# Kernel optimization log

Hardware: AMD Instinct MI355X
Metric: run time of the kernel (lower is better)

Reference implementation:

```python
import jax, jax.numpy as jnp
import numpy as np

D_MODEL = 1024
N_HEADS = 16
D_FF = 4096
LN_EPS = 1e-5


def _layer_norm(x, g, b):
    m = jnp.mean(x, axis=-1, keepdims=True)
    v = jnp.mean((x - m) ** 2, axis=-1, keepdims=True)
    return (x - m) / jnp.sqrt(v + LN_EPS) * g + b


def setup_inputs() -> dict:
    key = jax.random.key(0)
    ks = jax.random.split(key, 16)
    s = 0.02
    d, dff = D_MODEL, D_FF
    return {
        "x": jax.random.normal(ks[0], (8, 1000, d), dtype=jnp.float32),
        # weights stored as (d_in, d_out); applied via x @ W
        "wq": jax.random.normal(ks[1], (d, d), dtype=jnp.float32) * s,
        "wk": jax.random.normal(ks[2], (d, d), dtype=jnp.float32) * s,
        "wv": jax.random.normal(ks[3], (d, d), dtype=jnp.float32) * s,
        "wo": jax.random.normal(ks[4], (d, d), dtype=jnp.float32) * s,
        "bo": jnp.zeros((d,), dtype=jnp.float32),
        "w1": jax.random.normal(ks[5], (d, dff), dtype=jnp.float32) * s,
        "b1": jnp.zeros((dff,), dtype=jnp.float32),
        "w2": jax.random.normal(ks[6], (dff, d), dtype=jnp.float32) * s,
        "b2": jnp.zeros((d,), dtype=jnp.float32),
        "g1": jnp.ones((d,), dtype=jnp.float32),
        "beta1": jnp.zeros((d,), dtype=jnp.float32),
        "g2": jnp.ones((d,), dtype=jnp.float32),
        "beta2": jnp.zeros((d,), dtype=jnp.float32),
    }


def reference(x, wq, wk, wv, wo, bo, w1, b1, w2, b2, g1, beta1, g2, beta2):
    B, S, D = x.shape
    H = N_HEADS
    dk = D // H

    # --- pre-norm attention ---
    h = _layer_norm(x, g1, beta1)
    q = (h @ wq).reshape(B, S, H, dk)
    k = (h @ wk).reshape(B, S, H, dk)
    v = (h @ wv).reshape(B, S, H, dk)
    scores = jnp.einsum('bqhd,bkhd->bhqk', q, k) / jnp.sqrt(jnp.float32(dk))
    mask = jnp.tril(jnp.ones((S, S), dtype=bool))  # causal
    scores = jnp.where(mask, scores, -jnp.inf)
    attn = jax.nn.softmax(scores, axis=-1)
    attended = jnp.einsum('bhqk,bkhd->bqhd', attn, v).reshape(B, S, D)
    x = x + attended @ wo + bo

    # --- pre-norm FFN (exact GELU, matching torch F.gelu default) ---
    h2 = _layer_norm(x, g2, beta2)
    ff = jax.nn.gelu(h2 @ w1 + b1, approximate=False) @ w2 + b2
    return x + ff
```

## Files before the change

### kernel.cpp

```cpp
#include <hip/hip_runtime.h>
#include <hip/hip_bf16.h>
#include <math.h>

#define D_MODEL 1024
#define D_FF    4096
#define N_HEADS 16
#define SEQ     1000
#define BATCH   8
#define M_TOK   (BATCH * SEQ)

typedef __bf16 bf16x8_t __attribute__((ext_vector_type(8)));
typedef short  short8_t __attribute__((ext_vector_type(8)));
typedef float  f32x4_t  __attribute__((ext_vector_type(4)));

__device__ __forceinline__ f32x4_t mfma_bf16(short8_t a, short8_t b, f32x4_t c) {
    return __builtin_amdgcn_mfma_f32_16x16x32_bf16(
        __builtin_bit_cast(bf16x8_t, a), __builtin_bit_cast(bf16x8_t, b), c, 0, 0, 0);
}

__device__ __forceinline__ unsigned short f2bf(float f) {
    union { float f; unsigned u; } x; x.f = f;
    unsigned r = (x.u + 0x7fffu + ((x.u >> 16) & 1u)) >> 16;
    return (unsigned short)r;
}

__device__ __forceinline__ float gelu_fast(float v) {
    float z = 1.5957691216f * v * fmaf(0.044715f, v * v, 1.0f);
    float e = __expf(-z);
    return v * __builtin_amdgcn_rcpf(1.0f + e);
}

__device__ __forceinline__ void gload_lds16(const void* g, void* l) {
    __builtin_amdgcn_global_load_lds(
        (const __attribute__((address_space(1))) unsigned int*)g,
        (__attribute__((address_space(3))) unsigned int*)l, 16, 0, 0);
}

__global__ __launch_bounds__(256) void wtrans4_kernel(
    const float* __restrict__ wa, const float* __restrict__ wb,
    const float* __restrict__ wc, const float* __restrict__ wd,
    unsigned short* __restrict__ oa, unsigned short* __restrict__ ob,
    unsigned short* __restrict__ oc, unsigned short* __restrict__ od) {
    __shared__ float tile[32][33];
    int z = blockIdx.z;
    const float* w = z == 0 ? wa : z == 1 ? wb : z == 2 ? wc : wd;
    unsigned short* wt = z == 0 ? oa : z == 1 ? ob : z == 2 ? oc : od;
    int n0 = blockIdx.x * 32, k0 = blockIdx.y * 32;
    int tx = threadIdx.x, ty = threadIdx.y;
#pragma unroll
    for (int i = 0; i < 4; ++i)
        tile[ty + i * 8][tx] = w[(size_t)(k0 + ty + i * 8) * D_MODEL + n0 + tx];
    __syncthreads();
#pragma unroll
    for (int i = 0; i < 4; ++i)
        wt[(size_t)(n0 + ty + i * 8) * D_MODEL + k0 + tx] = f2bf(tile[tx][ty + i * 8]);
}

__global__ __launch_bounds__(256) void wtrans_kernel(const float* __restrict__ w,
                                                     unsigned short* __restrict__ wt,
                                                     int Kd, int Nd) {
    __shared__ float tile[32][33];
    int n0 = blockIdx.x * 32, k0 = blockIdx.y * 32;
    int tx = threadIdx.x, ty = threadIdx.y;
#pragma unroll
    for (int i = 0; i < 4; ++i)
        tile[ty + i * 8][tx] = w[(size_t)(k0 + ty + i * 8) * Nd + n0 + tx];
    __syncthreads();
#pragma unroll
    for (int i = 0; i < 4; ++i)
        wt[(size_t)(n0 + ty + i * 8) * Kd + k0 + tx] = f2bf(tile[tx][ty + i * 8]);
}

__global__ __launch_bounds__(256) void vtrans_kernel(const unsigned short* __restrict__ v,
                                                     unsigned short* __restrict__ vt) {
    __shared__ unsigned short tile[32][33];
    int b = blockIdx.z;
    int c0 = blockIdx.x * 32, s0 = blockIdx.y * 32;
    int tx = threadIdx.x, ty = threadIdx.y;
#pragma unroll
    for (int i = 0; i < 4; ++i) {
        int s = s0 + ty + i * 8;
        unsigned short val = 0;
        if (s < SEQ) val = v[((size_t)b * SEQ + s) * D_MODEL + c0 + tx];
        tile[ty + i * 8][tx] = val;
    }
    __syncthreads();
#pragma unroll
    for (int i = 0; i < 4; ++i) {
        int c = c0 + ty + i * 8;
        vt[((size_t)b * D_MODEL + c) * 1024 + s0 + tx] = tile[tx][ty + i * 8];
    }
}

__global__ __launch_bounds__(256) void ln_kernel(const float* __restrict__ x,
                                                 const float* __restrict__ g,
                                                 const float* __restrict__ beta,
                                                 unsigned short* __restrict__ out) {
    int row = blockIdx.x, tid = threadIdx.x;
    const float4 v = ((const float4*)(x + (size_t)row * D_MODEL))[tid];
    float s  = v.x + v.y + v.z + v.w;
    float s2 = v.x * v.x + v.y * v.y + v.z * v.z + v.w * v.w;
#pragma unroll
    for (int o = 32; o > 0; o >>= 1) { s += __shfl_xor(s, o, 64); s2 += __shfl_xor(s2, o, 64); }
    __shared__ float red[8];
    int wave = tid >> 6, lane = tid & 63;
    if (lane == 0) { red[wave] = s; red[wave + 4] = s2; }
    __syncthreads();
    s  = red[0] + red[1] + red[2] + red[3];
    s2 = red[4] + red[5] + red[6] + red[7];
    float mean = s * (1.0f / D_MODEL);
    float var  = s2 * (1.0f / D_MODEL) - mean * mean;
    float rstd = rsqrtf(var + 1e-5f);
    float4 gg = ((const float4*)g)[tid];
    float4 bb = ((const float4*)beta)[tid];
    ushort4 o4;
    o4.x = f2bf((v.x - mean) * rstd * gg.x + bb.x);
    o4.y = f2bf((v.y - mean) * rstd * gg.y + bb.y);
    o4.z = f2bf((v.z - mean) * rstd * gg.z + bb.z);
    o4.w = f2bf((v.w - mean) * rstd * gg.w + bb.w);
    ((ushort4*)(out + (size_t)row * D_MODEL))[tid] = o4;
}

enum { EPI_BF16 = 0, EPI_GELU = 1, EPI_RES_F32 = 2 };

template <int EPI, int KDIM, bool FUSE3>
__global__ __launch_bounds__(256) void gemm_bt(
    const unsigned short* __restrict__ A,
    const unsigned short* __restrict__ Bt0,
    const unsigned short* __restrict__ Bt1,
    const unsigned short* __restrict__ Bt2,
    const float* __restrict__ bias,
    const float* __restrict__ resid,
    void* __restrict__ out0, void* out1, void* out2,
    int Mdim, int Ndim) {
    constexpr int K = KDIM;
    __shared__ unsigned short lda[128 * 64];
    __shared__ unsigned short ldb[128 * 64];
    int tid = threadIdx.x;
    int lane = tid & 63, wave = tid >> 6;
    int l15 = lane & 15, quad = lane >> 4;
    int rt = blockIdx.y * 128;
    const unsigned short* Bt = Bt0;
    void* outp = out0;
    int ct;
    if (FUSE3) {
        int sel = blockIdx.x >> 3;
        ct = (blockIdx.x & 7) * 128;
        Bt   = sel == 0 ? Bt0  : (sel == 1 ? Bt1  : Bt2);
        outp = sel == 0 ? out0 : (sel == 1 ? out1 : out2);
    } else {
        ct = blockIdx.x * 128;
    }
    int wr = (wave >> 1) * 64, wc = (wave & 1) * 64;
    f32x4_t acc[4][4] = {};

    const unsigned short* ag[4];
    const unsigned short* bg[4];
#pragma unroll
    for (int i = 0; i < 4; ++i) {
        int gidx = tid + i * 256;
        int row = gidx >> 3, cp = gidx & 7;
        int c = cp ^ (row & 7);
        int ar = rt + row; if (ar >= Mdim) ar = Mdim - 1;
        ag[i] = A  + (size_t)ar * K + c * 8;
        bg[i] = Bt + (size_t)(ct + row) * K + c * 8;
    }

    for (int kt = 0; kt < K / 64; ++kt) {
        __syncthreads();
#pragma unroll
        for (int i = 0; i < 4; ++i) {
            gload_lds16(ag[i], (char*)lda + (wave * 64 + i * 256) * 16);
            gload_lds16(bg[i], (char*)ldb + (wave * 64 + i * 256) * 16);
            ag[i] += 64; bg[i] += 64;
        }
        __syncthreads();
#pragma unroll
        for (int kc = 0; kc < 2; ++kc) {
            short8_t af[4], bfr[4];
#pragma unroll
            for (int mi = 0; mi < 4; ++mi) {
                int ra = wr + mi * 16 + l15;
                int cg = (kc * 4 + quad) ^ (ra & 7);
                af[mi] = *(const short8_t*)(lda + (ra * 8 + cg) * 8);
            }
#pragma unroll
            for (int ni = 0; ni < 4; ++ni) {
                int rb = wc + ni * 16 + l15;
                int cg = (kc * 4 + quad) ^ (rb & 7);
                bfr[ni] = *(const short8_t*)(ldb + (rb * 8 + cg) * 8);
            }
#pragma unroll
            for (int mi = 0; mi < 4; ++mi)
#pragma unroll
                for (int ni = 0; ni < 4; ++ni)
                    acc[mi][ni] = mfma_bf16(af[mi], bfr[ni], acc[mi][ni]);
        }
    }

    float bias_c[4];
    if (EPI != EPI_BF16) {
#pragma unroll
        for (int ni = 0; ni < 4; ++ni) bias_c[ni] = bias[ct + wc + ni * 16 + l15];
    }

#pragma unroll
    for (int mi = 0; mi < 4; ++mi) {
#pragma unroll
        for (int r = 0; r < 4; ++r) {
            int grow = rt + wr + mi * 16 + quad * 4 + r;
            if (grow >= Mdim) continue;
#pragma unroll
            for (int ni = 0; ni < 4; ++ni) {
                int gcol = ct + wc + ni * 16 + l15;
                float v = acc[mi][ni][r];
                size_t idx = (size_t)grow * Ndim + gcol;
                if (EPI == EPI_BF16) {
                    ((unsigned short*)outp)[idx] = f2bf(v);
                } else if (EPI == EPI_GELU) {
                    v += bias_c[ni];
                    ((unsigned short*)outp)[idx] = f2bf(gelu_fast(v));
                } else {
                    v += bias_c[ni] + resid[idx];
                    ((float*)outp)[idx] = v;
                }
            }
        }
    }
}

__global__ __launch_bounds__(256) void attn_kernel(
    const unsigned short* __restrict__ q,
    const unsigned short* __restrict__ k,
    const unsigned short* __restrict__ vt,
    unsigned short* __restrict__ att) {
    int qt = blockIdx.x, h = blockIdx.y, b = blockIdx.z;
    int tid = threadIdx.x, lane = tid & 63, wave = tid >> 6;
    int l15 = lane & 15, quad = lane >> 4;
    __shared__ unsigned short kt_lds[64 * 72];
    __shared__ unsigned short vt_lds[64 * 72];
    __shared__ unsigned short p_lds[4][16 * 72];
    int qbase = qt * 64 + wave * 16;

    short8_t aq[2];
    {
        int qr = qbase + l15; if (qr > SEQ - 1) qr = SEQ - 1;
        const unsigned short* qp = q + ((size_t)(b * SEQ + qr)) * D_MODEL + h * 64 + quad * 8;
        aq[0] = *(const short8_t*)qp;
        aq[1] = *(const short8_t*)(qp + 32);
    }
    f32x4_t o[4] = {};
    float m_run[4], l_run[4];
#pragma unroll
    for (int r = 0; r < 4; ++r) { m_run[r] = -3.0e38f; l_run[r] = 0.f; }

    for (int ktile = 0; ktile <= qt; ++ktile) {
        __syncthreads();
#pragma unroll
        for (int i = 0; i < 2; ++i) {
            int gidx = tid + i * 256;
            int row = gidx >> 3, c = gidx & 7;
            int key = ktile * 64 + row; if (key > SEQ - 1) key = SEQ - 1;
            short8_t kv = *(const short8_t*)(k + ((size_t)(b * SEQ + key)) * D_MODEL + h * 64 + c * 8);
            *(short8_t*)(kt_lds + row * 72 + c * 8) = kv;
            short8_t vv = *(const short8_t*)(vt + ((size_t)((b * N_HEADS + h) * 64 + row)) * 1024 + ktile * 64 + c * 8);
            *(short8_t*)(vt_lds + row * 72 + c * 8) = vv;
        }
        __syncthreads();

        f32x4_t s[4];
#pragma unroll
        for (int nb = 0; nb < 4; ++nb) {
            f32x4_t z = {};
#pragma unroll
            for (int kc = 0; kc < 2; ++kc) {
                short8_t bk = *(const short8_t*)(kt_lds + (nb * 16 + l15) * 72 + kc * 32 + quad * 8);
                z = mfma_bf16(aq[kc], bk, z);
            }
            s[nb] = z;
        }
        float sc[4][4];
#pragma unroll
        for (int nb = 0; nb < 4; ++nb) {
            int kg = ktile * 64 + nb * 16 + l15;
#pragma unroll
            for (int r = 0; r < 4; ++r) {
                int qg = qbase + quad * 4 + r;
                float v = s[nb][r] * 0.125f;
                sc[nb][r] = (kg <= qg && kg < SEQ) ? v : -1e30f;
            }
        }
        float rmax[4], rsum[4], alpha[4];
#pragma unroll
        for (int r = 0; r < 4; ++r)
            rmax[r] = fmaxf(fmaxf(sc[0][r], sc[1][r]), fmaxf(sc[2][r], sc[3][r]));
#pragma unroll
        for (int ofs = 1; ofs < 16; ofs <<= 1)
#pragma unroll
            for (int r = 0; r < 4; ++r)
                rmax[r] = fmaxf(rmax[r], __shfl_xor(rmax[r], ofs, 64));
#pragma unroll
        for (int r = 0; r < 4; ++r) {
            float nm = fmaxf(m_run[r], rmax[r]);
            alpha[r] = __expf(m_run[r] - nm);
            m_run[r] = nm;
            rsum[r] = 0.f;
        }
#pragma unroll
        for (int nb = 0; nb < 4; ++nb)
#pragma unroll
            for (int r = 0; r < 4; ++r) {
                float p = __expf(sc[nb][r] - m_run[r]);
                sc[nb][r] = p;
                rsum[r] += p;
            }
#pragma unroll
        for (int ofs = 1; ofs < 16; ofs <<= 1)
#pragma unroll
            for (int r = 0; r < 4; ++r)
                rsum[r] += __shfl_xor(rsum[r], ofs, 64);
#pragma unroll
        for (int r = 0; r < 4; ++r)
            l_run[r] = l_run[r] * alpha[r] + rsum[r];
#pragma unroll
        for (int db = 0; db < 4; ++db)
#pragma unroll
            for (int r = 0; r < 4; ++r)
                o[db][r] *= alpha[r];
        unsigned short* pw = p_lds[wave];
#pragma unroll
        for (int nb = 0; nb < 4; ++nb)
#pragma unroll
            for (int r = 0; r < 4; ++r)
                pw[(quad * 4 + r) * 72 + nb * 16 + l15] = f2bf(sc[nb][r]);
        asm volatile("s_waitcnt lgkmcnt(0)" ::: "memory");
        short8_t ap[2];
        ap[0] = *(const short8_t*)(pw + l15 * 72 + quad * 8);
        ap[1] = *(const short8_t*)(pw + l15 * 72 + 32 + quad * 8);
#pragma unroll
        for (int db = 0; db < 4; ++db)
#pragma unroll
            for (int kc = 0; kc < 2; ++kc) {
                short8_t bv = *(const short8_t*)(vt_lds + (db * 16 + l15) * 72 + kc * 32 + quad * 8);
                o[db] = mfma_bf16(ap[kc], bv, o[db]);
            }
    }
#pragma unroll
    for (int r = 0; r < 4; ++r) {
        int qg = qbase + quad * 4 + r;
        if (qg >= SEQ) continue;
        float inv = __builtin_amdgcn_rcpf(l_run[r]);
#pragma unroll
        for (int db = 0; db < 4; ++db)
            att[((size_t)(b * SEQ + qg)) * D_MODEL + h * 64 + db * 16 + l15] = f2bf(o[db][r] * inv);
    }
}

extern "C" void kernel_launch(void* const* d_in, const int* in_sizes, int n_in,
                              void* d_out, int out_size, void* d_ws, size_t ws_size,
                              hipStream_t stream) {
    const float* x     = (const float*)d_in[0];
    const float* wq    = (const float*)d_in[1];
    const float* wk    = (const float*)d_in[2];
    const float* wv    = (const float*)d_in[3];
    const float* wo    = (const float*)d_in[4];
    const float* bo    = (const float*)d_in[5];
    const float* w1    = (const float*)d_in[6];
    const float* b1    = (const float*)d_in[7];
    const float* w2    = (const float*)d_in[8];
    const float* b2    = (const float*)d_in[9];
    const float* g1    = (const float*)d_in[10];
    const float* beta1 = (const float*)d_in[11];
    const float* g2    = (const float*)d_in[12];
    const float* beta2 = (const float*)d_in[13];
    float* out = (float*)d_out;
    char* ws = (char*)d_ws;

    const size_t SZ_MD_BF16 = (size_t)M_TOK * D_MODEL * 2;
    unsigned short* h1  = (unsigned short*)(ws);
    unsigned short* qb  = (unsigned short*)(ws + SZ_MD_BF16);
    unsigned short* kb  = (unsigned short*)(ws + 2 * SZ_MD_BF16);
    unsigned short* vb  = (unsigned short*)(ws + 3 * SZ_MD_BF16);
    unsigned short* atb = (unsigned short*)(ws + 4 * SZ_MD_BF16);
    unsigned short* ffb = qb;
    size_t off = 5 * SZ_MD_BF16;
    unsigned short* vtb = (unsigned short*)(ws + off); off += (size_t)BATCH * D_MODEL * 1024 * 2;
    float* x1 = (float*)(ws + off); off += (size_t)M_TOK * D_MODEL * 4;
    unsigned short* wqt = (unsigned short*)(ws + off); off += (size_t)D_MODEL * D_MODEL * 2;
    unsigned short* wkt = (unsigned short*)(ws + off); off += (size_t)D_MODEL * D_MODEL * 2;
    unsigned short* wvt = (unsigned short*)(ws + off); off += (size_t)D_MODEL * D_MODEL * 2;
    unsigned short* wot = (unsigned short*)(ws + off); off += (size_t)D_MODEL * D_MODEL * 2;
    unsigned short* w1t = (unsigned short*)(ws + off); off += (size_t)D_MODEL * D_FF * 2;
    unsigned short* w2t = (unsigned short*)(ws + off); off += (size_t)D_MODEL * D_FF * 2;

    dim3 tb(32, 8);
    wtrans4_kernel<<<dim3(32, 32, 4), tb, 0, stream>>>(wq, wk, wv, wo, wqt, wkt, wvt, wot);
    wtrans_kernel<<<dim3(128, 32), tb, 0, stream>>>(w1, w1t, D_MODEL, D_FF);
    wtrans_kernel<<<dim3(32, 128), tb, 0, stream>>>(w2, w2t, D_FF, D_MODEL);

    ln_kernel<<<M_TOK, 256, 0, stream>>>(x, g1, beta1, h1);

    const int MT = (M_TOK + 127) / 128;
    gemm_bt<EPI_BF16, D_MODEL, true><<<dim3(24, MT), 256, 0, stream>>>(
        h1, wqt, wkt, wvt, nullptr, nullptr, qb, kb, vb, M_TOK, D_MODEL);

    vtrans_kernel<<<dim3(32, 32, 8), tb, 0, stream>>>(vb, vtb);

    attn_kernel<<<dim3(16, N_HEADS, BATCH), 256, 0, stream>>>(qb, kb, vtb, atb);

    gemm_bt<EPI_RES_F32, D_MODEL, false><<<dim3(8, MT), 256, 0, stream>>>(
        atb, wot, nullptr, nullptr, bo, x, x1, nullptr, nullptr, M_TOK, D_MODEL);

    ln_kernel<<<M_TOK, 256, 0, stream>>>(x1, g2, beta2, h1);

    gemm_bt<EPI_GELU, D_MODEL, false><<<dim3(32, MT), 256, 0, stream>>>(
        h1, w1t, nullptr, nullptr, b1, nullptr, ffb, nullptr, nullptr, M_TOK, D_FF);

    gemm_bt<EPI_RES_F32, D_FF, false><<<dim3(8, MT), 256, 0, stream>>>(
        ffb, w2t, nullptr, nullptr, b2, x1, out, nullptr, nullptr, M_TOK, D_MODEL);
}
```

Measured before the change: 570.4 us.

## Restructure causal attention: 128-query blocks, swizzled LDS, direct global-to-LDS loads

Each wave of the attention kernel now handles 32 queries in two 16-row groups instead of 16, so every K and V fragment read from LDS is reused twice, and the grid is halved. K and V tiles are staged with direct global-to-LDS 16-byte loads into XOR-swizzled unpadded LDS. Scores are computed transposed (K as the A operand), so each lane holds a whole query row and the row max and sum need only two cross-lane shuffles instead of four. The P tile is written as packed 64-bit stores. The cost is more registers per wave and coarser blocks, which may worsen causal load imbalance and occupancy.

```diff
diff --git a/kernel.cpp b/kernel.cpp
--- a/kernel.cpp
+++ b/kernel.cpp
@@ -237,122 +237,150 @@
     int qt = blockIdx.x, h = blockIdx.y, b = blockIdx.z;
     int tid = threadIdx.x, lane = tid & 63, wave = tid >> 6;
     int l15 = lane & 15, quad = lane >> 4;
-    __shared__ unsigned short kt_lds[64 * 72];
-    __shared__ unsigned short vt_lds[64 * 72];
-    __shared__ unsigned short p_lds[4][16 * 72];
-    int qbase = qt * 64 + wave * 16;
-
-    short8_t aq[2];
-    {
-        int qr = qbase + l15; if (qr > SEQ - 1) qr = SEQ - 1;
+    __shared__ unsigned short kt_lds[64 * 64];
+    __shared__ unsigned short vt_lds[64 * 64];
+    __shared__ unsigned short p_lds[4][32 * 64];
+    unsigned short* pw = p_lds[wave];
+    int qw = qt * 128 + wave * 32;
+
+    short8_t aq[2][2];
+#pragma unroll
+    for (int g = 0; g < 2; ++g) {
+        int qr = qw + g * 16 + l15; if (qr > SEQ - 1) qr = SEQ - 1;
         const unsigned short* qp = q + ((size_t)(b * SEQ + qr)) * D_MODEL + h * 64 + quad * 8;
-        aq[0] = *(const short8_t*)qp;
-        aq[1] = *(const short8_t*)(qp + 32);
-    }
-    f32x4_t o[4] = {};
-    float m_run[4], l_run[4];
-#pragma unroll
-    for (int r = 0; r < 4; ++r) { m_run[r] = -3.0e38f; l_run[r] = 0.f; }
-
-    for (int ktile = 0; ktile <= qt; ++ktile) {
+        aq[g][0] = *(const short8_t*)qp;
+        aq[g][1] = *(const short8_t*)(qp + 32);
+    }
+    f32x4_t o[2][4] = {};
+    float m_run[2] = {-3.0e38f, -3.0e38f};
+    float l_run[2] = {0.f, 0.f};
+
+    int ntiles = 2 * qt + 2;
+    for (int ktile = 0; ktile < ntiles; ++ktile) {
         __syncthreads();
 #pragma unroll
         for (int i = 0; i < 2; ++i) {
-            int gidx = tid + i * 256;
-            int row = gidx >> 3, c = gidx & 7;
-            int key = ktile * 64 + row; if (key > SEQ - 1) key = SEQ - 1;
-            short8_t kv = *(const short8_t*)(k + ((size_t)(b * SEQ + key)) * D_MODEL + h * 64 + c * 8);
-            *(short8_t*)(kt_lds + row * 72 + c * 8) = kv;
-            short8_t vv = *(const short8_t*)(vt + ((size_t)((b * N_HEADS + h) * 64 + row)) * 1024 + ktile * 64 + c * 8);
-            *(short8_t*)(vt_lds + row * 72 + c * 8) = vv;
+            int g2 = wave * 64 + (lane) + i * 256;
+            int row = g2 >> 3, cp = g2 & 7;
+            int c = cp ^ (row & 7);
+            int key = ktile * 64 + row; int keyc = key < SEQ ? key : SEQ - 1;
+            gload_lds16(k + ((size_t)(b * SEQ + keyc)) * D_MODEL + h * 64 + c * 8,
+                        (char*)kt_lds + (size_t)(wave * 64 + i * 256) * 16);
+            gload_lds16(vt + ((size_t)((b * N_HEADS + h) * 64 + row)) * 1024 + ktile * 64 + c * 8,
+                        (char*)vt_lds + (size_t)(wave * 64 + i * 256) * 16);
         }
         __syncthreads();
 
-        f32x4_t s[4];
-#pragma unroll
-        for (int nb = 0; nb < 4; ++nb) {
-            f32x4_t z = {};
+        if (ktile * 64 > qw + 31) continue;
+
+        short8_t kf[4][2];
+#pragma unroll
+        for (int nb = 0; nb < 4; ++nb)
 #pragma unroll
             for (int kc = 0; kc < 2; ++kc) {
-                short8_t bk = *(const short8_t*)(kt_lds + (nb * 16 + l15) * 72 + kc * 32 + quad * 8);
-                z = mfma_bf16(aq[kc], bk, z);
-            }
-            s[nb] = z;
-        }
-        float sc[4][4];
-#pragma unroll
-        for (int nb = 0; nb < 4; ++nb) {
-            int kg = ktile * 64 + nb * 16 + l15;
+                int row = nb * 16 + l15;
+                kf[nb][kc] = *(const short8_t*)(kt_lds + (row * 8 + ((kc * 4 + quad) ^ (row & 7))) * 8);
+            }
+
+        bool gact[2];
+#pragma unroll
+        for (int g = 0; g < 2; ++g) {
+            gact[g] = (ktile * 64 <= qw + g * 16 + 15);
+            if (!gact[g]) continue;
+            f32x4_t s[4] = {};
+#pragma unroll
+            for (int nb = 0; nb < 4; ++nb)
+#pragma unroll
+                for (int kc = 0; kc < 2; ++kc)
+                    s[nb] = mfma_bf16(kf[nb][kc], aq[g][kc], s[nb]);
+            int qrow = qw + g * 16 + l15;
+            float sc[4][4];
+#pragma unroll
+            for (int nb = 0; nb < 4; ++nb)
+#pragma unroll
+                for (int r = 0; r < 4; ++r) {
+                    int key = ktile * 64 + nb * 16 + quad * 4 + r;
+                    float v = s[nb][r] * 0.125f;
+                    sc[nb][r] = (key <= qrow) ? v : -1e30f;
+                }
+            float mx = sc[0][0];
+#pragma unroll
+            for (int nb = 0; nb < 4; ++nb)
+#pragma unroll
+                for (int r = 0; r < 4; ++r) mx = fmaxf(mx, sc[nb][r]);
+            mx = fmaxf(mx, __shfl_xor(mx, 16, 64));
+            mx = fmaxf(mx, __shfl_xor(mx, 32, 64));
+            float mnew = fmaxf(m_run[g], mx);
+            float alpha = __expf(m_run[g] - mnew);
+            m_run[g] = mnew;
+            float rs = 0.f;
+#pragma unroll
+            for (int nb = 0; nb < 4; ++nb)
+#pragma unroll
+                for (int r = 0; r < 4; ++r) {
+                    float p = __expf(sc[nb][r] - mnew);
+                    sc[nb][r] = p;
+                    rs += p;
+                }
+            rs += __shfl_xor(rs, 16, 64);
+            rs += __shfl_xor(rs, 32, 64);
+            l_run[g] = l_run[g] * alpha + rs;
 #pragma unroll
             for (int r = 0; r < 4; ++r) {
-                int qg = qbase + quad * 4 + r;
-                float v = s[nb][r] * 0.125f;
-                sc[nb][r] = (kg <= qg && kg < SEQ) ? v : -1e30f;
-            }
-        }
-        float rmax[4], rsum[4], alpha[4];
-#pragma unroll
-        for (int r = 0; r < 4; ++r)
-            rmax[r] = fmaxf(fmaxf(sc[0][r], sc[1][r]), fmaxf(sc[2][r], sc[3][r]));
-#pragma unroll
-        for (int ofs = 1; ofs < 16; ofs <<= 1)
-#pragma unroll
-            for (int r = 0; r < 4; ++r)
-                rmax[r] = fmaxf(rmax[r], __shfl_xor(rmax[r], ofs, 64));
+                float a = __shfl(alpha, quad * 4 + r, 64);
+#pragma unroll
+                for (int db = 0; db < 4; ++db) o[g][db][r] *= a;
+            }
+#pragma unroll
+            for (int nb = 0; nb < 4; ++nb) {
+                unsigned long long pv =
+                    (unsigned long long)f2bf(sc[nb][0]) |
+                    ((unsigned long long)f2bf(sc[nb][1]) << 16) |
+                    ((unsigned long long)f2bf(sc[nb][2]) << 32) |
+                    ((unsigned long long)f2bf(sc[nb][3]) << 48);
+                int chunk = (4 * nb + quad) ^ ((l15 & 7) << 1);
+                *(unsigned long long*)(pw + (g * 16 + l15) * 64 + chunk * 4) = pv;
+            }
+        }
+        asm volatile("s_waitcnt lgkmcnt(0)" ::: "memory");
+
+        short8_t vf[4][2];
+#pragma unroll
+        for (int db = 0; db < 4; ++db)
+#pragma unroll
+            for (int kc = 0; kc < 2; ++kc) {
+                int row = db * 16 + l15;
+                vf[db][kc] = *(const short8_t*)(vt_lds + (row * 8 + ((kc * 4 + quad) ^ (row & 7))) * 8);
+            }
+#pragma unroll
+        for (int g = 0; g < 2; ++g) {
+            if (!gact[g]) continue;
+            short8_t ap[2];
+#pragma unroll
+            for (int kc = 0; kc < 2; ++kc)
+                ap[kc] = *(const short8_t*)(pw + (g * 16 + l15) * 64 +
+                                            ((kc * 4 + quad) ^ (l15 & 7)) * 8);
+#pragma unroll
+            for (int db = 0; db < 4; ++db)
+#pragma unroll
+                for (int kc = 0; kc < 2; ++kc)
+                    o[g][db] = mfma_bf16(ap[kc], vf[db][kc], o[g][db]);
+        }
+    }
+
+#pragma unroll
+    for (int g = 0; g < 2; ++g) {
+        float linv = __builtin_amdgcn_rcpf(l_run[g]);
 #pragma unroll
         for (int r = 0; r < 4; ++r) {
-            float nm = fmaxf(m_run[r], rmax[r]);
-            alpha[r] = __expf(m_run[r] - nm);
-            m_run[r] = nm;
-            rsum[r] = 0.f;
-        }
-#pragma unroll
-        for (int nb = 0; nb < 4; ++nb)
-#pragma unroll
-            for (int r = 0; r < 4; ++r) {
-                float p = __expf(sc[nb][r] - m_run[r]);
-                sc[nb][r] = p;
-                rsum[r] += p;
-            }
-#pragma unroll
-        for (int ofs = 1; ofs < 16; ofs <<= 1)
-#pragma unroll
-            for (int r = 0; r < 4; ++r)
-                rsum[r] += __shfl_xor(rsum[r], ofs, 64);
-#pragma unroll
-        for (int r = 0; r < 4; ++r)
-            l_run[r] = l_run[r] * alpha[r] + rsum[r];
-#pragma unroll
-        for (int db = 0; db < 4; ++db)
-#pragma unroll
-            for (int r = 0; r < 4; ++r)
-                o[db][r] *= alpha[r];
-        unsigned short* pw = p_lds[wave];
-#pragma unroll
-        for (int nb = 0; nb < 4; ++nb)
-#pragma unroll
-            for (int r = 0; r < 4; ++r)
-                pw[(quad * 4 + r) * 72 + nb * 16 + l15] = f2bf(sc[nb][r]);
-        asm volatile("s_waitcnt lgkmcnt(0)" ::: "memory");
-        short8_t ap[2];
-        ap[0] = *(const short8_t*)(pw + l15 * 72 + quad * 8);
-        ap[1] = *(const short8_t*)(pw + l15 * 72 + 32 + quad * 8);
-#pragma unroll
-        for (int db = 0; db < 4; ++db)
-#pragma unroll
-            for (int kc = 0; kc < 2; ++kc) {
-                short8_t bv = *(const short8_t*)(vt_lds + (db * 16 + l15) * 72 + kc * 32 + quad * 8);
-                o[db] = mfma_bf16(ap[kc], bv, o[db]);
-            }
-    }
-#pragma unroll
-    for (int r = 0; r < 4; ++r) {
-        int qg = qbase + quad * 4 + r;
-        if (qg >= SEQ) continue;
-        float inv = __builtin_amdgcn_rcpf(l_run[r]);
-#pragma unroll
-        for (int db = 0; db < 4; ++db)
-            att[((size_t)(b * SEQ + qg)) * D_MODEL + h * 64 + db * 16 + l15] = f2bf(o[db][r] * inv);
+            float nr = __shfl(linv, quad * 4 + r, 64);
+            int qg = qw + g * 16 + quad * 4 + r;
+            if (qg >= SEQ) continue;
+#pragma unroll
+            for (int db = 0; db < 4; ++db)
+                att[((size_t)(b * SEQ + qg)) * D_MODEL + h * 64 + db * 16 + l15] =
+                    f2bf(o[g][db][r] * nr);
+        }
     }
 }
 
@@ -406,7 +434,7 @@
 
     vtrans_kernel<<<dim3(32, 32, 8), tb, 0, stream>>>(vb, vtb);
 
-    attn_kernel<<<dim3(16, N_HEADS, BATCH), 256, 0, stream>>>(qb, kb, vtb, atb);
+    attn_kernel<<<dim3(8, N_HEADS, BATCH), 256, 0, stream>>>(qb, kb, vtb, atb);
 
     gemm_bt<EPI_RES_F32, D_MODEL, false><<<dim3(8, MT), 256, 0, stream>>>(
         atb, wot, nullptr, nullptr, bo, x, x1, nullptr, nullptr, M_TOK, D_MODEL);
```

After: 520.5 us. 8.7% less time.
